# Optimization experiments

Measured on AMD Instinct MI355X. Metric: run time of the kernel, lower is better.

Reference implementation:

```python
import jax, jax.numpy as jnp
import numpy as np

B, S, H, NH = 2, 2048, 2048, 16
HD = H // NH


def setup_inputs() -> dict:
    key = jax.random.key(0)
    ks = jax.random.split(key, 10)
    s = 1.0 / np.sqrt(H)
    x = jax.random.normal(ks[0], (B, S, H), dtype=jnp.float32)
    # additive causal mask: 0 on/below diagonal, -1e9 above
    causal = jnp.tril(jnp.ones((S, S), dtype=bool))
    mask = jnp.where(causal, 0.0, -1e9).astype(jnp.float32)[None, None]
    return {
        "x": x,
        "mask": mask,
        "wq": jax.random.normal(ks[1], (H, H), jnp.float32) * s,
        "bq": jnp.zeros((H,), jnp.float32),
        "wk": jax.random.normal(ks[2], (H, H), jnp.float32) * s,
        "bk": jnp.zeros((H,), jnp.float32),
        "wv": jax.random.normal(ks[3], (H, H), jnp.float32) * s,
        "bv": jnp.zeros((H,), jnp.float32),
        "wo": jax.random.normal(ks[4], (H, H), jnp.float32) * s,
        "bo": jnp.zeros((H,), jnp.float32),
    }


def reference(x, mask, wq, bq, wk, bk, wv, bv, wo, bo):
    b, s, _ = x.shape
    scale = HD ** (-0.5)
    # projections -> [b, nh, s, hd]
    def split_heads(t):
        return t.reshape(b, s, NH, HD).transpose(0, 2, 1, 3)
    q = split_heads(x @ wq + bq)
    k = split_heads(x @ wk + bk)
    v = split_heads(x @ wv + bv)
    scores = jnp.einsum('bhqd,bhkd->bhqk', q, k) * scale + mask
    attn = jax.nn.softmax(scores, axis=-1)
    out = jnp.einsum('bhqk,bhkd->bhqd', attn, v)
    out = out.transpose(0, 2, 1, 3).reshape(b, s, H)
    return out @ wo + bo
```

## Files before the change

### kernel.cpp

```cpp
#include <hip/hip_runtime.h>


using bf16x8 = __attribute__((ext_vector_type(8))) short;
using bf16x4 = __attribute__((ext_vector_type(4))) short;
using f32x4  = __attribute__((ext_vector_type(4))) float;

#define S_LEN 2048
#define NHEAD 16
#define HDIM  128
#define HID   2048

__device__ __forceinline__ unsigned short f2bf(float f) {
    unsigned int u = __float_as_uint(f);
    u += 0x7fffu + ((u >> 16) & 1u);
    return (unsigned short)(u >> 16);
}
__device__ __forceinline__ void gl2lds16(const void* g, void* l) {
    __builtin_amdgcn_global_load_lds(
        (const __attribute__((address_space(1))) void*)g,
        (__attribute__((address_space(3))) void*)l, 16, 0, 0);
}

__device__ __forceinline__ f32x4 pv_mfma(bf16x4 a, bf16x4 b, f32x4 c) {
#if defined(__HIP_DEVICE_COMPILE__)
#if __has_builtin(__builtin_amdgcn_mfma_f32_16x16x16bf16_1k)
    return __builtin_amdgcn_mfma_f32_16x16x16bf16_1k(a, b, c, 0, 0, 0);
#else
    asm("v_mfma_f32_16x16x16_bf16 %0, %1, %2, %0" : "+v"(c) : "v"(a), "v"(b));
    return c;
#endif
#else
    (void)a; (void)b;
    return c;
#endif
}

__global__ void convert_all(const float* __restrict__ x,
                            const float* __restrict__ w0, const float* __restrict__ w1,
                            const float* __restrict__ w2, const float* __restrict__ w3,
                            unsigned short* __restrict__ xb,
                            unsigned short* __restrict__ t0, unsigned short* __restrict__ t1,
                            unsigned short* __restrict__ t2, unsigned short* __restrict__ t3) {
    int z = blockIdx.z;
    if (z >= 4) {
        int lin = (z - 4) * 1024 + blockIdx.y * 32 + blockIdx.x;
        int i = (lin * 256 + threadIdx.x) * 4;
        float4 v = *(const float4*)(x + i);
        ushort4 o;
        o.x = f2bf(v.x); o.y = f2bf(v.y); o.z = f2bf(v.z); o.w = f2bf(v.w);
        *(ushort4*)(xb + i) = o;
        return;
    }
    __shared__ float tile[64][65];
    const float* src = (z == 0) ? w0 : (z == 1) ? w1 : (z == 2) ? w2 : w3;
    unsigned short* dst = (z == 0) ? t0 : (z == 1) ? t1 : (z == 2) ? t2 : t3;
    int r0 = blockIdx.y * 64, c0 = blockIdx.x * 64;
    int t = threadIdx.x;
    for (int i = t; i < 64 * 64; i += 256) {
        int r = i >> 6, c = i & 63;
        tile[r][c] = src[(size_t)(r0 + r) * HID + c0 + c];
    }
    __syncthreads();
    for (int i = t; i < 64 * 64; i += 256) {
        int r = i & 63, c = i >> 6;
        dst[(size_t)(c0 + c) * HID + r0 + r] = f2bf(tile[r][c]);
    }
}

__device__ __forceinline__ void sched0() { __builtin_amdgcn_sched_barrier(0); }
__device__ __forceinline__ void w_lgkm4() { asm volatile("s_waitcnt lgkmcnt(4)" ::: "memory"); sched0(); }
__device__ __forceinline__ void w_lgkm0() { asm volatile("s_waitcnt lgkmcnt(0)" ::: "memory"); sched0(); }
template <int NJ> __device__ __forceinline__ void w_lgkm_4nj() {
    if constexpr (NJ == 3) { asm volatile("s_waitcnt lgkmcnt(7)" ::: "memory"); }
    else                   { asm volatile("s_waitcnt lgkmcnt(6)" ::: "memory"); }
    sched0();
}
template <int NJ> __device__ __forceinline__ void w_vm_ns() {
    if constexpr (NJ == 3) { asm volatile("s_waitcnt vmcnt(7)" ::: "memory"); }
    else                   { asm volatile("s_waitcnt vmcnt(6)" ::: "memory"); }
    sched0();
}
__device__ __forceinline__ void w_vm4() { asm volatile("s_waitcnt vmcnt(4)" ::: "memory"); sched0(); }
__device__ __forceinline__ void w_vm2() { asm volatile("s_waitcnt vmcnt(2)" ::: "memory"); sched0(); }
__device__ __forceinline__ void w_vm0() { asm volatile("s_waitcnt vmcnt(0)" ::: "memory"); sched0(); }
__device__ __forceinline__ void barx() {
    asm volatile("" ::: "memory");
    __builtin_amdgcn_s_barrier();
    asm volatile("" ::: "memory");
}

__launch_bounds__(512, 2)
__global__ void gemm8q(const unsigned short* __restrict__ A,
                       const unsigned short* __restrict__ Bt,
                       const float* __restrict__ bias0,
                       const float* __restrict__ bias1,
                       const float* __restrict__ bias2,
                       unsigned short* __restrict__ C0,
                       unsigned short* __restrict__ C1,
                       unsigned short* __restrict__ C2) {
    __shared__ __align__(16) unsigned short lds[57344];
    unsigned short* const A0 = lds;
    unsigned short* const A1 = lds + 16384;
    unsigned short* const B0 = lds + 32768;
    unsigned short* const B1 = lds + 45056;

    int vb = (blockIdx.x & 7) * 64 + (blockIdx.x >> 3);
    int m0  = (vb & 15) * 256;
    int n0g = (vb >> 4) * 192;

    int tid = threadIdx.x;
    int lane = tid & 63;
    int wv_ = tid >> 6;
    int wr = wv_ >> 2, wc = wv_ & 3;
    int l15 = lane & 15, quad = lane >> 4;

    int tr = tid >> 3;
    int tc = ((tid & 7) ^ (tr & 7)) << 3;
    const unsigned short* gA = A  + (size_t)(m0  + tr) * HID + tc;
    const unsigned short* gB = Bt + (size_t)(n0g + tr) * HID + tc;
    const int td8 = tid * 8;

    int arow0 = (wr * 64 + l15) * 64;
    int brow0 = (wc * 48 + l15) * 64;
    int swz[2] = { ((quad ^ (l15 & 7)) << 3), (((4 + quad) ^ (l15 & 7)) << 3) };

    f32x4 acc[8][3];
#pragma unroll
    for (int i = 0; i < 8; ++i)
#pragma unroll
        for (int j = 0; j < 3; ++j) acc[i][j] = (f32x4){0.f, 0.f, 0.f, 0.f};

    bf16x8 av[4];
    bf16x8 bv[2][3];

#define SGA(kt, half, AD) do {                                               \
    size_t _g = (size_t)((half) * 128) * HID + (size_t)(kt) * 64;            \
    gl2lds16(gA + _g,            (AD) + (half) * 8192 + td8);                \
    gl2lds16(gA + _g + 64 * HID, (AD) + (half) * 8192 + 4096 + td8); } while (0)

#define SGB3(kt, third, BD) do {                                             \
    size_t _g = (size_t)((third) * 64) * HID + (size_t)(kt) * 64;            \
    gl2lds16(gB + _g, (BD) + (third) * 4096 + td8); } while (0)

#define RDA(AD, hm, kk) do {                                                 \
    _Pragma("unroll")                                                        \
    for (int mi = 0; mi < 4; ++mi)                                           \
        av[mi] = *(const bf16x8*)((AD) + arow0 + (hm) * 8192                 \
                                  + mi * 1024 + swz[kk]); } while (0)

#define RDB(BD, kk) do {                                                     \
    _Pragma("unroll")                                                        \
    for (int nj = 0; nj < 3; ++nj)                                           \
        bv[kk][nj] = *(const bf16x8*)((BD) + brow0 + nj * 1024 + swz[kk]); } while (0)

#define MFQ(hm, kk) do {                                                     \
    __builtin_amdgcn_s_setprio(1);                                           \
    _Pragma("unroll")                                                        \
    for (int mi = 0; mi < 4; ++mi)                                           \
        _Pragma("unroll")                                                    \
        for (int nj = 0; nj < 3; ++nj)                                       \
            acc[(hm) * 4 + mi][nj] =                                         \
                __builtin_amdgcn_mfma_f32_16x16x32_bf16(av[mi], bv[kk][nj],  \
                    acc[(hm) * 4 + mi][nj], 0, 0, 0);                        \
    __builtin_amdgcn_s_setprio(0); sched0(); } while (0)

    SGA(0, 0, A0); SGA(0, 1, A0);
    SGB3(0, 0, B0); SGB3(0, 1, B0); SGB3(0, 2, B0);
    SGA(1, 0, A1); SGB3(1, 0, B1); SGB3(1, 1, B1);
    w_vm4();
    barx();

    for (int it = 0; it < 16; ++it) {
        int t  = 2 * it;
        int t2 = (t + 2 < 32) ? t + 2 : 31;
        int t3 = (t + 3 < 32) ? t + 3 : 31;
        RDA(A0, 0, 0); RDB(B0, 0);
        SGA(t + 1, 1, A1); SGB3(t + 1, 2, B1);
        barx(); w_lgkm0();
        MFQ(0, 0);
        barx();
        RDA(A0, 0, 1); RDB(B0, 1);
        barx(); w_lgkm0();
        MFQ(0, 1);
        barx();
        RDA(A0, 1, 0);
        SGA(t2, 0, A0);
        barx(); w_lgkm0();
        MFQ(1, 0);
        barx();
        RDA(A0, 1, 1);
        SGB3(t2, 0, B0); SGB3(t2, 1, B0);
        barx(); w_lgkm0();
        MFQ(1, 1);
        w_vm4();
        barx();
        RDA(A1, 0, 0); RDB(B1, 0);
        SGA(t2, 1, A0); SGB3(t2, 2, B0);
        barx(); w_lgkm0();
        MFQ(0, 0);
        barx();
        RDA(A1, 0, 1); RDB(B1, 1);
        barx(); w_lgkm0();
        MFQ(0, 1);
        barx();
        RDA(A1, 1, 0);
        SGA(t3, 0, A1);
        barx(); w_lgkm0();
        MFQ(1, 0);
        barx();
        RDA(A1, 1, 1);
        SGB3(t3, 0, B1); SGB3(t3, 1, B1);
        barx(); w_lgkm0();
        MFQ(1, 1);
        w_vm4();
        barx();
    }
    asm volatile("s_waitcnt vmcnt(0) lgkmcnt(0)" ::: "memory");

#undef SGA
#undef SGB3
#undef RDA
#undef RDB
#undef MFQ

#pragma unroll
    for (int j = 0; j < 3; ++j) {
        int n = n0g + wc * 48 + j * 16 + l15;
        int zj = n >> 11;
        int nn = n & 2047;
        float bn = (zj == 0) ? bias0[nn] : (zj == 1) ? bias1[nn] : bias2[nn];
        unsigned short* Cz = (zj == 0) ? C0 : (zj == 1) ? C1 : C2;
#pragma unroll
        for (int i = 0; i < 8; ++i) {
            int mb = m0 + (i >> 2) * 128 + wr * 64 + (i & 3) * 16 + quad * 4;
            if (zj == 2) {
                int b = mb >> 11, s = mb & 2047, h = nn >> 7, d = nn & 127;
                int kt = s >> 4, qv = (s >> 2) & 3, ct = d >> 4, lv = d & 15;
                size_t addr = ((((size_t)((b << 4) + h) * 128 + kt) * 4 + (ct >> 1)) * 4 + qv) * 128
                              + lv * 8 + (ct & 1) * 4;
                ushort4 o;
                o.x = f2bf(acc[i][j][0] + bn);
                o.y = f2bf(acc[i][j][1] + bn);
                o.z = f2bf(acc[i][j][2] + bn);
                o.w = f2bf(acc[i][j][3] + bn);
                *(ushort4*)&Cz[addr] = o;
            } else {
#pragma unroll
                for (int reg = 0; reg < 4; ++reg) {
                    int m = mb + reg;
                    float v = acc[i][j][reg] + bn;
                    int b = m >> 11, s = m & 2047, h = nn >> 7, d = nn & 127;
                    if (zj == 1) {
                        int kt = s >> 4, lk = s & 15, kk = d >> 5, qk = (d >> 3) & 3, e = d & 7;
                        size_t addr = ((((size_t)((b << 4) + h) * 128 + kt) * 4 + kk) * 4 + qk) * 128
                                      + lk * 8 + e;
                        Cz[addr] = f2bf(v);
                    } else {
                        Cz[(size_t)(((b << 4) + h) * S_LEN + s) * HDIM + d] = f2bf(v);
                    }
                }
            }
        }
    }
}

template <int MODE, int NJ>
__launch_bounds__(512, 2)
__global__ void gemmT(const unsigned short* __restrict__ A,
                      const unsigned short* __restrict__ Bt0,
                      const float* __restrict__ bias0,
                      float* __restrict__ Cf) {
    __shared__ __align__(16) unsigned short lds[2 * 16384 + 2 * NJ * 4096];
    unsigned short* const A0 = lds;
    unsigned short* const A1 = lds + 16384;
    unsigned short* const B0 = lds + 32768;
    unsigned short* const B1 = lds + 32768 + NJ * 4096;

    int vb = (blockIdx.x & 7) * 32 + (blockIdx.x >> 3);
    int m0  = (vb & 15) * 256;
    int n0g = (vb >> 4) * (NJ * 64);

    int tid = threadIdx.x;
    int lane = tid & 63;
    int wv_ = tid >> 6;
    int wr = wv_ >> 2, wc = wv_ & 3;
    int l15 = lane & 15, quad = lane >> 4;

    int tr = tid >> 3;
    int tc = ((tid & 7) ^ (tr & 7)) << 3;
    const unsigned short* gA = A   + (size_t)(m0  + tr) * HID + tc;
    const unsigned short* gB = Bt0 + (size_t)(n0g + tr) * HID + tc;
    const int td8 = tid * 8;

    int arow0 = (wr * 128 + l15) * 64;
    int brow0 = (wc * (16 * NJ) + l15) * 64;
    int sw0 = ((quad ^ (l15 & 7)) << 3);
    int sw1 = (((4 + quad) ^ (l15 & 7)) << 3);

    f32x4 acc[8][NJ];
#pragma unroll
    for (int i = 0; i < 8; ++i)
#pragma unroll
        for (int j = 0; j < NJ; ++j) acc[i][j] = (f32x4){0.f, 0.f, 0.f, 0.f};

    bf16x8 aX[4], aY[4], b0v[NJ], b1v[NJ];

#define STAGE(kt, AD, BD) do { int _kc = (kt) * 64;                          \
    gl2lds16(gA + _kc,             (AD) + td8);                              \
    gl2lds16(gA + 64 * HID + _kc,  (AD) + 4096 + td8);                       \
    gl2lds16(gA + 128 * HID + _kc, (AD) + 8192 + td8);                       \
    gl2lds16(gA + 192 * HID + _kc, (AD) + 12288 + td8);                      \
    _Pragma("unroll")                                                        \
    for (int _r = 0; _r < NJ; ++_r)                                          \
        gl2lds16(gB + (size_t)(_r * 64) * HID + _kc, (BD) + _r * 4096 + td8); } while (0)

#define LDA4(dst, AD, QB, SW) do {                                           \
    dst[0] = *(const bf16x8*)((AD) + arow0 + ((QB) + 0) * 1024 + (SW));      \
    dst[1] = *(const bf16x8*)((AD) + arow0 + ((QB) + 1) * 1024 + (SW));      \
    dst[2] = *(const bf16x8*)((AD) + arow0 + ((QB) + 2) * 1024 + (SW));      \
    dst[3] = *(const bf16x8*)((AD) + arow0 + ((QB) + 3) * 1024 + (SW)); } while (0)

#define LDB(dst, BD, SW) do {                                                \
    _Pragma("unroll")                                                        \
    for (int _n = 0; _n < NJ; ++_n)                                          \
        dst[_n] = *(const bf16x8*)((BD) + brow0 + _n * 1024 + (SW)); } while (0)

#define MF(Q, a, b) do {                                                     \
    __builtin_amdgcn_s_setprio(1);                                           \
    _Pragma("unroll")                                                        \
    for (int mi = 0; mi < 4; ++mi)                                           \
        _Pragma("unroll")                                                    \
        for (int nj = 0; nj < NJ; ++nj)                                      \
            acc[(Q) * 4 + mi][nj] =                                          \
                __builtin_amdgcn_mfma_f32_16x16x32_bf16(a[mi], b[nj],        \
                                                        acc[(Q) * 4 + mi][nj], 0, 0, 0); \
    __builtin_amdgcn_s_setprio(0); } while (0)

#define TILE(AD, BD, AN, BN_, ks) do {                                       \
    LDA4(aY, AD, 4, sw0);                                                    \
    w_lgkm4();                                                               \
    MF(0, aX, b0v);                                                          \
    LDA4(aX, AD, 0, sw1);                                                    \
    LDB(b1v, BD, sw1);                                                       \
    w_lgkm_4nj<NJ>();                                                        \
    MF(1, aY, b0v);                                                          \
    LDA4(aY, AD, 4, sw1);                                                    \
    w_lgkm4();                                                               \
    MF(0, aX, b1v);                                                          \
    w_lgkm0();                                                               \
    barx();                                                                  \
    STAGE(ks, AD, BD);                                                       \
    w_vm_ns<NJ>();                                                           \
    barx();                                                                  \
    LDA4(aX, AN, 0, sw0);                                                    \
    LDB(b0v, BN_, sw0);                                                      \
    sched0();                                                                \
    MF(1, aY, b1v);                                                          \
} while (0)

    STAGE(0, A0, B0);
    STAGE(1, A1, B1);
    w_vm_ns<NJ>();
    barx();
    LDA4(aX, A0, 0, sw0);
    LDB(b0v, B0, sw0);

    for (int t = 0; t < 32; t += 2) {
        TILE(A0, B0, A1, B1, (t + 2 < 32) ? t + 2 : 31);
        TILE(A1, B1, A0, B0, (t + 3 < 32) ? t + 3 : 31);
    }
    asm volatile("s_waitcnt vmcnt(0) lgkmcnt(0)" ::: "memory");

#undef TILE
#undef STAGE
#undef LDA4
#undef LDB
#undef MF

#pragma unroll
    for (int j = 0; j < NJ; ++j) {
        int n = n0g + wc * (16 * NJ) + j * 16 + l15;
        float bn = bias0[n];
#pragma unroll
        for (int i = 0; i < 8; ++i) {
            int mb = m0 + wr * 128 + i * 16 + quad * 4;
#pragma unroll
            for (int reg = 0; reg < 4; ++reg) {
                int m = mb + reg;
                Cf[(size_t)m * HID + n] = acc[i][j][reg] + bn;
            }
        }
    }
}

__launch_bounds__(256, 2)
__global__ void attn_kernel(const unsigned short* __restrict__ Qg,
                            const unsigned short* __restrict__ Kp,
                            const unsigned short* __restrict__ Vp,
                            unsigned short* __restrict__ O) {
    __shared__ __align__(16) unsigned short kv[2][4096];

    int linear = blockIdx.x;
    int xcd = linear & 7;
    int u = linear >> 3;
    int bh = xcd * 4 + (u & 3);
    int q = u >> 2;
    int b = bh >> 4, h = bh & 15;

    int tid = threadIdx.x, lane = tid & 63, w = tid >> 6;
    int l15 = lane & 15, quad = lane >> 4;

    const unsigned short* Qb = Qg + (size_t)bh * (S_LEN * HDIM);
    const unsigned short* Kg = Kp + (size_t)bh * 262144;
    const unsigned short* Vg = Vp + (size_t)bh * 262144;
    const float k2 = 0.08838834764831845f * 1.4426950408889634f;

    const int frag = quad * 128 + l15 * 8;
    const int td8 = tid * 8;

#define VLO(x) __builtin_shufflevector(x, x, 0, 1, 2, 3)
#define VHI(x) __builtin_shufflevector(x, x, 4, 5, 6, 7)
#define ASTAGE(kt, bf) do { size_t _g = (size_t)(kt) * 2048 + td8;             \
    gl2lds16(Kg + _g, &kv[bf][td8]);                                           \
    gl2lds16(Vg + _g, &kv[bf][2048 + td8]); } while (0)

    auto run_qblock = [&](int qb) {
        int s  = 4 * qb + w;
        int r0 = s * 16;
        int N  = 4 * qb + 4;

        bf16x8 qf[4];
#pragma unroll
        for (int kk = 0; kk < 4; ++kk)
            qf[kk] = *(const bf16x8*)&Qb[(size_t)(r0 + l15) * HDIM + kk * 32 + quad * 8];

        f32x4 o_acc[8];
#pragma unroll
        for (int c = 0; c < 8; ++c) o_acc[c] = (f32x4){0.f, 0.f, 0.f, 0.f};
        float l_part = 0.f;

        ASTAGE(0, 0);
        for (int kt = 0; kt < N; ++kt) {
            int nk = (kt + 1 < N) ? kt + 1 : kt;
            ASTAGE(nk, (kt + 1) & 1);
            w_vm2();
            barx();

            const unsigned short* KL = &kv[kt & 1][frag];
            const unsigned short* VL = &kv[kt & 1][2048 + frag];
            bf16x8 kb0 = *(const bf16x8*)(KL);
            bf16x8 kb1 = *(const bf16x8*)(KL + 512);
            bf16x8 kb2 = *(const bf16x8*)(KL + 1024);
            bf16x8 kb3 = *(const bf16x8*)(KL + 1536);
            bf16x8 v0 = *(const bf16x8*)(VL);
            bf16x8 v1 = *(const bf16x8*)(VL + 512);
            bf16x8 v2 = *(const bf16x8*)(VL + 1024);
            bf16x8 v3 = *(const bf16x8*)(VL + 1536);

            f32x4 st0 = (f32x4){0.f, 0.f, 0.f, 0.f};
            f32x4 st1 = (f32x4){0.f, 0.f, 0.f, 0.f};
            __builtin_amdgcn_s_setprio(1);
            st0 = __builtin_amdgcn_mfma_f32_16x16x32_bf16(kb0, qf[0], st0, 0, 0, 0);
            st1 = __builtin_amdgcn_mfma_f32_16x16x32_bf16(kb1, qf[1], st1, 0, 0, 0);
            st0 = __builtin_amdgcn_mfma_f32_16x16x32_bf16(kb2, qf[2], st0, 0, 0, 0);
            st1 = __builtin_amdgcn_mfma_f32_16x16x32_bf16(kb3, qf[3], st1, 0, 0, 0);
            __builtin_amdgcn_s_setprio(0);
            f32x4 stv = st0 + st1;

            float p0, p1, p2, p3;
            int doff = kt - s;
            if (doff >= 0) {
                int d16 = doff << 4;
                p0 = (d16 + quad * 4 + 0 <= l15) ? exp2f(stv[0] * k2) : 0.f;
                p1 = (d16 + quad * 4 + 1 <= l15) ? exp2f(stv[1] * k2) : 0.f;
                p2 = (d16 + quad * 4 + 2 <= l15) ? exp2f(stv[2] * k2) : 0.f;
                p3 = (d16 + quad * 4 + 3 <= l15) ? exp2f(stv[3] * k2) : 0.f;
            } else {
                p0 = exp2f(stv[0] * k2); p1 = exp2f(stv[1] * k2);
                p2 = exp2f(stv[2] * k2); p3 = exp2f(stv[3] * k2);
            }
            l_part += (p0 + p1) + (p2 + p3);

            bf16x4 pf;
            pf[0] = (short)f2bf(p0); pf[1] = (short)f2bf(p1);
            pf[2] = (short)f2bf(p2); pf[3] = (short)f2bf(p3);

            __builtin_amdgcn_s_setprio(1);
            o_acc[0] = pv_mfma(pf, VLO(v0), o_acc[0]);
            o_acc[1] = pv_mfma(pf, VHI(v0), o_acc[1]);
            o_acc[2] = pv_mfma(pf, VLO(v1), o_acc[2]);
            o_acc[3] = pv_mfma(pf, VHI(v1), o_acc[3]);
            o_acc[4] = pv_mfma(pf, VLO(v2), o_acc[4]);
            o_acc[5] = pv_mfma(pf, VHI(v2), o_acc[5]);
            o_acc[6] = pv_mfma(pf, VLO(v3), o_acc[6]);
            o_acc[7] = pv_mfma(pf, VHI(v3), o_acc[7]);
            __builtin_amdgcn_s_setprio(0);
            barx();
        }
        w_vm0();
        barx();

        float lp = l_part;
        lp += __shfl_xor(lp, 16, 64);
        lp += __shfl_xor(lp, 32, 64);
#pragma unroll
        for (int reg = 0; reg < 4; ++reg) {
            float l = __shfl(lp, quad * 4 + reg, 64);
            float inv = 1.f / l;
            int srow = r0 + quad * 4 + reg;
            unsigned short* op = O + (size_t)(b * S_LEN + srow) * HID + h * HDIM;
#pragma unroll
            for (int ct = 0; ct < 8; ++ct)
                op[ct * 16 + l15] = f2bf(o_acc[ct][reg] * inv);
        }
    };

    run_qblock(q);
    run_qblock(31 - q);

#undef ASTAGE
#undef VLO
#undef VHI
}

extern "C" void kernel_launch(void* const* d_in, const int* in_sizes, int n_in,
                              void* d_out, int out_size, void* d_ws, size_t ws_size,
                              hipStream_t stream) {
    (void)in_sizes; (void)n_in; (void)out_size; (void)ws_size;
    const float* x  = (const float*)d_in[0];
    const float* wq = (const float*)d_in[2];
    const float* bq = (const float*)d_in[3];
    const float* wk = (const float*)d_in[4];
    const float* bk = (const float*)d_in[5];
    const float* wv = (const float*)d_in[6];
    const float* bv = (const float*)d_in[7];
    const float* wo = (const float*)d_in[8];
    const float* bo = (const float*)d_in[9];
    float* out = (float*)d_out;

    unsigned short* ws = (unsigned short*)d_ws;
    const size_t WSZ = 4194304;
    unsigned short* wqT = ws;
    unsigned short* wkT = ws + WSZ;
    unsigned short* wvT = ws + 2 * WSZ;
    unsigned short* woT = ws + 3 * WSZ;
    unsigned short* xb  = ws + 4 * WSZ;
    unsigned short* Ab  = ws + 4 * WSZ;
    unsigned short* Qb  = ws + 6 * WSZ;
    unsigned short* Kb  = ws + 8 * WSZ;
    unsigned short* Vb  = ws + 10 * WSZ;

    convert_all<<<dim3(32, 32, 12), 256, 0, stream>>>(x, wq, wk, wv, wo,
                                                      xb, wqT, wkT, wvT, woT);
    gemm8q<<<dim3(512), 512, 0, stream>>>(xb, wqT, bq, bk, bv, Qb, Kb, Vb);
    attn_kernel<<<dim3(512), 256, 0, stream>>>(Qb, Kb, Vb, Ab);
    gemmT<0, 2><<<dim3(256), 512, 0, stream>>>(Ab, woT, bo, out);
}
```

Baseline: 376.1 us.

## Rewrite output projection GEMM with 8-phase half-tile staged pipeline

Replaces the templated output-projection GEMM with a dedicated kernel that splits each K-tile into four phases (two M halves by two K sub-chunks). Global-to-LDS loads are issued in half-tile pieces interleaved between MFMA phases, and each phase is fenced by barriers. Warps now own interleaved 64-row strips in each 128-row half instead of a contiguous 128-row block. The aim is finer-grained overlap of memory staging with compute, at the cost of many more barriers and full lgkm waits per tile.

```diff
diff --git a/kernel.cpp b/kernel.cpp
--- a/kernel.cpp
+++ b/kernel.cpp
@@ -68,19 +68,9 @@
 }
 
 __device__ __forceinline__ void sched0() { __builtin_amdgcn_sched_barrier(0); }
-__device__ __forceinline__ void w_lgkm4() { asm volatile("s_waitcnt lgkmcnt(4)" ::: "memory"); sched0(); }
 __device__ __forceinline__ void w_lgkm0() { asm volatile("s_waitcnt lgkmcnt(0)" ::: "memory"); sched0(); }
-template <int NJ> __device__ __forceinline__ void w_lgkm_4nj() {
-    if constexpr (NJ == 3) { asm volatile("s_waitcnt lgkmcnt(7)" ::: "memory"); }
-    else                   { asm volatile("s_waitcnt lgkmcnt(6)" ::: "memory"); }
-    sched0();
-}
-template <int NJ> __device__ __forceinline__ void w_vm_ns() {
-    if constexpr (NJ == 3) { asm volatile("s_waitcnt vmcnt(7)" ::: "memory"); }
-    else                   { asm volatile("s_waitcnt vmcnt(6)" ::: "memory"); }
-    sched0();
-}
 __device__ __forceinline__ void w_vm4() { asm volatile("s_waitcnt vmcnt(4)" ::: "memory"); sched0(); }
+__device__ __forceinline__ void w_vm3() { asm volatile("s_waitcnt vmcnt(3)" ::: "memory"); sched0(); }
 __device__ __forceinline__ void w_vm2() { asm volatile("s_waitcnt vmcnt(2)" ::: "memory"); sched0(); }
 __device__ __forceinline__ void w_vm0() { asm volatile("s_waitcnt vmcnt(0)" ::: "memory"); sched0(); }
 __device__ __forceinline__ void barx() {
@@ -264,21 +254,20 @@
     }
 }
 
-template <int MODE, int NJ>
 __launch_bounds__(512, 2)
-__global__ void gemmT(const unsigned short* __restrict__ A,
-                      const unsigned short* __restrict__ Bt0,
-                      const float* __restrict__ bias0,
-                      float* __restrict__ Cf) {
-    __shared__ __align__(16) unsigned short lds[2 * 16384 + 2 * NJ * 4096];
+__global__ void gemm8o(const unsigned short* __restrict__ A,
+                       const unsigned short* __restrict__ Bt,
+                       const float* __restrict__ bias0,
+                       float* __restrict__ Cf) {
+    __shared__ __align__(16) unsigned short lds[49152];
     unsigned short* const A0 = lds;
     unsigned short* const A1 = lds + 16384;
     unsigned short* const B0 = lds + 32768;
-    unsigned short* const B1 = lds + 32768 + NJ * 4096;
+    unsigned short* const B1 = lds + 40960;
 
     int vb = (blockIdx.x & 7) * 32 + (blockIdx.x >> 3);
     int m0  = (vb & 15) * 256;
-    int n0g = (vb >> 4) * (NJ * 64);
+    int n0g = (vb >> 4) * 128;
 
     int tid = threadIdx.x;
     int lane = tid & 63;
@@ -288,102 +277,120 @@
 
     int tr = tid >> 3;
     int tc = ((tid & 7) ^ (tr & 7)) << 3;
-    const unsigned short* gA = A   + (size_t)(m0  + tr) * HID + tc;
-    const unsigned short* gB = Bt0 + (size_t)(n0g + tr) * HID + tc;
+    const unsigned short* gA = A  + (size_t)(m0  + tr) * HID + tc;
+    const unsigned short* gB = Bt + (size_t)(n0g + tr) * HID + tc;
     const int td8 = tid * 8;
 
-    int arow0 = (wr * 128 + l15) * 64;
-    int brow0 = (wc * (16 * NJ) + l15) * 64;
-    int sw0 = ((quad ^ (l15 & 7)) << 3);
-    int sw1 = (((4 + quad) ^ (l15 & 7)) << 3);
-
-    f32x4 acc[8][NJ];
+    int arow0 = (wr * 64 + l15) * 64;
+    int brow0 = (wc * 32 + l15) * 64;
+    int swz[2] = { ((quad ^ (l15 & 7)) << 3), (((4 + quad) ^ (l15 & 7)) << 3) };
+
+    f32x4 acc[8][2];
 #pragma unroll
     for (int i = 0; i < 8; ++i)
 #pragma unroll
-        for (int j = 0; j < NJ; ++j) acc[i][j] = (f32x4){0.f, 0.f, 0.f, 0.f};
-
-    bf16x8 aX[4], aY[4], b0v[NJ], b1v[NJ];
-
-#define STAGE(kt, AD, BD) do { int _kc = (kt) * 64;                          \
-    gl2lds16(gA + _kc,             (AD) + td8);                              \
-    gl2lds16(gA + 64 * HID + _kc,  (AD) + 4096 + td8);                       \
-    gl2lds16(gA + 128 * HID + _kc, (AD) + 8192 + td8);                       \
-    gl2lds16(gA + 192 * HID + _kc, (AD) + 12288 + td8);                      \
+        for (int j = 0; j < 2; ++j) acc[i][j] = (f32x4){0.f, 0.f, 0.f, 0.f};
+
+    bf16x8 av[4];
+    bf16x8 bv[2][2];
+
+#define SGA(kt, half, AD) do {                                               \
+    size_t _g = (size_t)((half) * 128) * HID + (size_t)(kt) * 64;            \
+    gl2lds16(gA + _g,            (AD) + (half) * 8192 + td8);                \
+    gl2lds16(gA + _g + 64 * HID, (AD) + (half) * 8192 + 4096 + td8); } while (0)
+
+#define SGB2(kt, half, BD) do {                                              \
+    size_t _g = (size_t)((half) * 64) * HID + (size_t)(kt) * 64;             \
+    gl2lds16(gB + _g, (BD) + (half) * 4096 + td8); } while (0)
+
+#define RDA(AD, hm, kk) do {                                                 \
     _Pragma("unroll")                                                        \
-    for (int _r = 0; _r < NJ; ++_r)                                          \
-        gl2lds16(gB + (size_t)(_r * 64) * HID + _kc, (BD) + _r * 4096 + td8); } while (0)
-
-#define LDA4(dst, AD, QB, SW) do {                                           \
-    dst[0] = *(const bf16x8*)((AD) + arow0 + ((QB) + 0) * 1024 + (SW));      \
-    dst[1] = *(const bf16x8*)((AD) + arow0 + ((QB) + 1) * 1024 + (SW));      \
-    dst[2] = *(const bf16x8*)((AD) + arow0 + ((QB) + 2) * 1024 + (SW));      \
-    dst[3] = *(const bf16x8*)((AD) + arow0 + ((QB) + 3) * 1024 + (SW)); } while (0)
-
-#define LDB(dst, BD, SW) do {                                                \
+    for (int mi = 0; mi < 4; ++mi)                                           \
+        av[mi] = *(const bf16x8*)((AD) + arow0 + (hm) * 8192                 \
+                                  + mi * 1024 + swz[kk]); } while (0)
+
+#define RDB(BD, kk) do {                                                     \
     _Pragma("unroll")                                                        \
-    for (int _n = 0; _n < NJ; ++_n)                                          \
-        dst[_n] = *(const bf16x8*)((BD) + brow0 + _n * 1024 + (SW)); } while (0)
-
-#define MF(Q, a, b) do {                                                     \
+    for (int nj = 0; nj < 2; ++nj)                                           \
+        bv[kk][nj] = *(const bf16x8*)((BD) + brow0 + nj * 1024 + swz[kk]); } while (0)
+
+#define MFQ(hm, kk) do {                                                     \
     __builtin_amdgcn_s_setprio(1);                                           \
     _Pragma("unroll")                                                        \
     for (int mi = 0; mi < 4; ++mi)                                           \
         _Pragma("unroll")                                                    \
-        for (int nj = 0; nj < NJ; ++nj)                                      \
-            acc[(Q) * 4 + mi][nj] =                                          \
-                __builtin_amdgcn_mfma_f32_16x16x32_bf16(a[mi], b[nj],        \
-                                                        acc[(Q) * 4 + mi][nj], 0, 0, 0); \
-    __builtin_amdgcn_s_setprio(0); } while (0)
-
-#define TILE(AD, BD, AN, BN_, ks) do {                                       \
-    LDA4(aY, AD, 4, sw0);                                                    \
-    w_lgkm4();                                                               \
-    MF(0, aX, b0v);                                                          \
-    LDA4(aX, AD, 0, sw1);                                                    \
-    LDB(b1v, BD, sw1);                                                       \
-    w_lgkm_4nj<NJ>();                                                        \
-    MF(1, aY, b0v);                                                          \
-    LDA4(aY, AD, 4, sw1);                                                    \
-    w_lgkm4();                                                               \
-    MF(0, aX, b1v);                                                          \
-    w_lgkm0();                                                               \
-    barx();                                                                  \
-    STAGE(ks, AD, BD);                                                       \
-    w_vm_ns<NJ>();                                                           \
-    barx();                                                                  \
-    LDA4(aX, AN, 0, sw0);                                                    \
-    LDB(b0v, BN_, sw0);                                                      \
-    sched0();                                                                \
-    MF(1, aY, b1v);                                                          \
-} while (0)
-
-    STAGE(0, A0, B0);
-    STAGE(1, A1, B1);
-    w_vm_ns<NJ>();
+        for (int nj = 0; nj < 2; ++nj)                                       \
+            acc[(hm) * 4 + mi][nj] =                                         \
+                __builtin_amdgcn_mfma_f32_16x16x32_bf16(av[mi], bv[kk][nj],  \
+                    acc[(hm) * 4 + mi][nj], 0, 0, 0);                        \
+    __builtin_amdgcn_s_setprio(0); sched0(); } while (0)
+
+    SGA(0, 0, A0); SGA(0, 1, A0);
+    SGB2(0, 0, B0); SGB2(0, 1, B0);
+    SGA(1, 0, A1); SGB2(1, 0, B1);
+    w_vm3();
     barx();
-    LDA4(aX, A0, 0, sw0);
-    LDB(b0v, B0, sw0);
-
-    for (int t = 0; t < 32; t += 2) {
-        TILE(A0, B0, A1, B1, (t + 2 < 32) ? t + 2 : 31);
-        TILE(A1, B1, A0, B0, (t + 3 < 32) ? t + 3 : 31);
+
+    for (int it = 0; it < 16; ++it) {
+        int t  = 2 * it;
+        int t2 = (t + 2 < 32) ? t + 2 : 31;
+        int t3 = (t + 3 < 32) ? t + 3 : 31;
+        RDA(A0, 0, 0); RDB(B0, 0);
+        SGA(t + 1, 1, A1); SGB2(t + 1, 1, B1);
+        barx(); w_lgkm0();
+        MFQ(0, 0);
+        barx();
+        RDA(A0, 0, 1); RDB(B0, 1);
+        barx(); w_lgkm0();
+        MFQ(0, 1);
+        barx();
+        RDA(A0, 1, 0);
+        SGA(t2, 0, A0);
+        barx(); w_lgkm0();
+        MFQ(1, 0);
+        barx();
+        RDA(A0, 1, 1);
+        SGB2(t2, 0, B0);
+        barx(); w_lgkm0();
+        MFQ(1, 1);
+        w_vm3();
+        barx();
+        RDA(A1, 0, 0); RDB(B1, 0);
+        SGA(t2, 1, A0); SGB2(t2, 1, B0);
+        barx(); w_lgkm0();
+        MFQ(0, 0);
+        barx();
+        RDA(A1, 0, 1); RDB(B1, 1);
+        barx(); w_lgkm0();
+        MFQ(0, 1);
+        barx();
+        RDA(A1, 1, 0);
+        SGA(t3, 0, A1);
+        barx(); w_lgkm0();
+        MFQ(1, 0);
+        barx();
+        RDA(A1, 1, 1);
+        SGB2(t3, 0, B1);
+        barx(); w_lgkm0();
+        MFQ(1, 1);
+        w_vm3();
+        barx();
     }
     asm volatile("s_waitcnt vmcnt(0) lgkmcnt(0)" ::: "memory");
 
-#undef TILE
-#undef STAGE
-#undef LDA4
-#undef LDB
-#undef MF
-
-#pragma unroll
-    for (int j = 0; j < NJ; ++j) {
-        int n = n0g + wc * (16 * NJ) + j * 16 + l15;
+#undef SGA
+#undef SGB2
+#undef RDA
+#undef RDB
+#undef MFQ
+
+#pragma unroll
+    for (int j = 0; j < 2; ++j) {
+        int n = n0g + wc * 32 + j * 16 + l15;
         float bn = bias0[n];
 #pragma unroll
         for (int i = 0; i < 8; ++i) {
-            int mb = m0 + wr * 128 + i * 16 + quad * 4;
+            int mb = m0 + (i >> 2) * 128 + wr * 64 + (i & 3) * 16 + quad * 4;
 #pragma unroll
             for (int reg = 0; reg < 4; ++reg) {
                 int m = mb + reg;
@@ -554,5 +561,5 @@
                                                       xb, wqT, wkT, wvT, woT);
     gemm8q<<<dim3(512), 512, 0, stream>>>(xb, wqT, bq, bk, bv, Qb, Kb, Vb);
     attn_kernel<<<dim3(512), 256, 0, stream>>>(Qb, Kb, Vb, Ab);
-    gemmT<0, 2><<<dim3(256), 512, 0, stream>>>(Ab, woT, bo, out);
-}
+    gemm8o<<<dim3(256), 512, 0, stream>>>(Ab, woT, bo, out);
+}
```

Result: no change. 375.6 us (-0.1%).
